# Kernel optimization log

Measured on AMD Instinct MI355X. Metric: run time of the kernel, lower is better.

Reference implementation:

```python
import jax, jax.numpy as jnp
import numpy as np

BS, D, N, E, L, NE = 8, 512, 2048, 8, 64, 524288


def conv1d_same(x, w, b):
    # x: [B, W, Cin], w: [K, Cin, Cout] -> [B, W, Cout], stride 1, 'same' padding
    y = jax.lax.conv_general_dilated(x, w, window_strides=(1,), padding='SAME',
                                     dimension_numbers=('NWC', 'WIO', 'NWC'))
    return y + b


def setup_inputs() -> dict:
    key = jax.random.key(0)
    ks = jax.random.split(key, 10)
    def nrm(k, shape, s=1.0):
        return jax.random.normal(k, shape, jnp.float32) * s
    return {
        'latent': nrm(ks[0], (BS, D)),
        'edge_index': jax.random.randint(ks[1], (2, NE), 0, BS * N),
        'W_dense': nrm(ks[2], (D, N), 0.05),
        'b_dense': jnp.zeros((N,), jnp.float32),
        'conv1_w': nrm(ks[3], (3, 1, E), 0.3),
        'conv1_b': jnp.zeros((E,), jnp.float32),
        'gat_Wq': nrm(ks[4], (E, E), 0.3),
        'gat_bq': jnp.zeros((E,), jnp.float32),
        'gat_Wk': nrm(ks[5], (E, E), 0.3),
        'gat_bk': jnp.zeros((E,), jnp.float32),
        'gat_Wv': nrm(ks[6], (E, E), 0.3),
        'gat_bias': jnp.zeros((E,), jnp.float32),
        'qkv_w': nrm(ks[7], (3, E, 3 * E * L), 0.1),
        'qkv_b': jnp.zeros((3 * E * L,), jnp.float32),
    }


def reference(latent, edge_index, W_dense, b_dense, conv1_w, conv1_b,
              gat_Wq, gat_bq, gat_Wk, gat_bk, gat_Wv, gat_bias, qkv_w, qkv_b):
    bs = latent.shape[0]
    # Dense -> [bs, N], expand -> Conv1D(E) -> [bs, N, E]
    skeleton = latent @ W_dense + b_dense
    skeleton = conv1d_same(skeleton[..., None], conv1_w, conv1_b)
    # concat(unstack, axis=0) == reshape to batched graph nodes [bs*N, E]
    x = skeleton.reshape(bs * N, E)
    BN = bs * N
    # GAT (tf_geometric, num_heads=1): add self-loops, per-edge dot-attention,
    # segment softmax over destination (row), scatter-sum aggregate.
    loops = jnp.arange(BN)
    row = jnp.concatenate([edge_index[0], loops])
    col = jnp.concatenate([edge_index[1], loops])
    Q = jax.nn.leaky_relu(x @ gat_Wq + gat_bq, 0.2)
    K = jax.nn.leaky_relu(x @ gat_Wk + gat_bk, 0.2)
    V = x @ gat_Wv
    score = jnp.sum(Q[row] * K[col], axis=-1)            # [n_edges + BN]
    smax = jax.ops.segment_max(score, row, num_segments=BN)
    ex = jnp.exp(score - smax[row])
    ssum = jax.ops.segment_sum(ex, row, num_segments=BN)
    alpha = ex / ssum[row]                               # segment softmax
    h = jax.ops.segment_sum(alpha[:, None] * V[col], row, num_segments=BN) + gat_bias
    graph = h.reshape(bs, N, E)                          # stack(split(., bs))
    # QVK conv over node axis -> [bs, N, 3*E*L]
    qvk = conv1d_same(graph, qkv_w, qkv_b)
    # stack(split(., L, -1), 1) then concat(unstack(., -2), -1)
    qvk = qvk.reshape(bs, N, L, 3 * E).transpose(0, 2, 1, 3).reshape(bs, L, N * 3 * E)
    q, v, k = jnp.split(qvk, 3, axis=-1)                 # each [bs, L, N*E]
    # keras Attention (use_scale=False): softmax(q @ k^T) @ v
    attn = jax.nn.softmax(jnp.einsum('btd,bsd->bts', q, k), axis=-1)
    seq = jnp.einsum('bts,bsd->btd', attn, v)
    # stack(split(., N, -1), -2) == reshape [bs, L, N, E]
    return seq.reshape(bs, L, N, E)
```

## Files before the change

### kernel.cpp

```cpp
#include <hip/hip_runtime.h>
#include <hip/hip_bf16.h>
#include <math.h>

#define BSZ 8
#define DDIM 512
#define NND 2048
#define EE 8
#define LLH 64
#define NEDGE 524288
#define BNN 16384
#define OCC 1536
#define DQ 16384

typedef __attribute__((ext_vector_type(8))) short short8;
typedef __attribute__((ext_vector_type(4))) unsigned short ushort4v;

__device__ inline unsigned short f2bf(float x) {
    __hip_bfloat16 h = __float2bfloat16(x);
    return __builtin_bit_cast(unsigned short, h);
}
__device__ inline float bf2f(unsigned short u) {
    return __uint_as_float(((unsigned int)u) << 16);
}

__device__ inline void gridbar64(int* c) {
    __syncthreads();
    if (threadIdx.x == 0) {
        __threadfence();
        atomicAdd(c, 1);
        while (atomicAdd(c, 0) < 64) __builtin_amdgcn_s_sleep(8);
        __threadfence();
    }
    __syncthreads();
}

__global__ __launch_bounds__(256) void k_densep(const float* __restrict__ latent,
                                                const float* __restrict__ Wd,
                                                float* __restrict__ pdense,
                                                int* __restrict__ hist,
                                                int* __restrict__ cbar) {
    int n0 = blockIdx.x * 32, d0 = blockIdx.y * 64;
    __shared__ float lat[8][64];
    int tid = threadIdx.x;
    if (blockIdx.y == 0) hist[blockIdx.x * 256 + tid] = 0;
    if (blockIdx.x == 0 && blockIdx.y == 0 && tid < 16) cbar[tid] = 0;
    #pragma unroll
    for (int r = 0; r < 2; ++r) {
        int i = r * 256 + tid;
        lat[i >> 6][i & 63] = latent[(i >> 6) * DDIM + d0 + (i & 63)];
    }
    __syncthreads();
    int nl = tid & 31, b = tid >> 5;
    const float* wp = Wd + (size_t)d0 * NND + n0 + nl;
    float acc = 0.f;
    #pragma unroll 8
    for (int d = 0; d < 64; ++d) acc += lat[b][d] * wp[(size_t)d * NND];
    pdense[((size_t)blockIdx.y * BSZ + b) * NND + n0 + nl] = acc;
}

__global__ __launch_bounds__(64) void k_gat(const float* __restrict__ pdense,
                                            const float* __restrict__ bd,
                                            const float* __restrict__ w1,
                                            const float* __restrict__ b1,
                                            const float* __restrict__ Wq, const float* __restrict__ bq,
                                            const float* __restrict__ Wk, const float* __restrict__ bk,
                                            const float* __restrict__ Wv,
                                            const int* __restrict__ ei,
                                            float* __restrict__ Qg, float* __restrict__ Kg,
                                            float* __restrict__ Vg, int* __restrict__ hist) {
    int i = blockIdx.x * 64 + threadIdx.x;
    int b = i >> 11, n = i & (NND - 1);
    float sm = 0.f, s0 = 0.f, sp = 0.f;
    #pragma unroll
    for (int ds = 0; ds < 8; ++ds) {
        const float* p = pdense + ((size_t)ds * BSZ + b) * NND + n;
        if (n > 0) sm += p[-1];
        s0 += p[0];
        if (n < NND - 1) sp += p[1];
    }
    if (n > 0) sm += bd[n - 1];
    s0 += bd[n];
    if (n < NND - 1) sp += bd[n + 1];
    float xr[EE];
    #pragma unroll
    for (int e = 0; e < EE; ++e)
        xr[e] = sm * w1[e] + s0 * w1[EE + e] + sp * w1[2 * EE + e] + b1[e];
    #pragma unroll
    for (int j = 0; j < EE; ++j) {
        float q = bq[j], k = bk[j], v = 0.f;
        #pragma unroll
        for (int c = 0; c < EE; ++c) {
            q += xr[c] * Wq[c * EE + j];
            k += xr[c] * Wk[c * EE + j];
            v += xr[c] * Wv[c * EE + j];
        }
        Qg[(size_t)i * EE + j] = (q >= 0.f) ? q : 0.2f * q;
        Kg[(size_t)i * EE + j] = (k >= 0.f) ? k : 0.2f * k;
        Vg[(size_t)i * EE + j] = v;
    }
    #pragma unroll 4
    for (int j = 0; j < 32; ++j)
        atomicAdd(hist + ei[i + j * BNN], 1);
}

__global__ __launch_bounds__(1024) void k_scan(const int* __restrict__ hist,
                                               int* __restrict__ offs,
                                               int* __restrict__ cnt) {
    int tid = threadIdx.x;
    int lane = tid & 63, wv = tid >> 6;
    const int4* hp = (const int4*)(hist + tid * 16);
    int4 a = hp[0], b4 = hp[1], c4 = hp[2], d4 = hp[3];
    int h[16] = {a.x, a.y, a.z, a.w, b4.x, b4.y, b4.z, b4.w,
                 c4.x, c4.y, c4.z, c4.w, d4.x, d4.y, d4.z, d4.w};
    int mysum = 0;
    #pragma unroll
    for (int i = 0; i < 16; ++i) mysum += h[i];
    int inc = mysum;
    #pragma unroll
    for (int off = 1; off < 64; off <<= 1) {
        int u = __shfl_up(inc, off, 64);
        if (lane >= off) inc += u;
    }
    __shared__ int wtot[16];
    if (lane == 63) wtot[wv] = inc;
    __syncthreads();
    if (tid < 16) {
        int t = wtot[tid];
        #pragma unroll
        for (int off = 1; off < 16; off <<= 1) {
            int u = __shfl_up(t, off, 16);
            if (tid >= off) t += u;
        }
        wtot[tid] = t;
    }
    __syncthreads();
    int run = (wv ? wtot[wv - 1] : 0) + inc - mysum;
    #pragma unroll
    for (int i = 0; i < 16; ++i) {
        offs[tid * 16 + i] = run;
        cnt[tid * 16 + i] = run;
        run += h[i];
    }
}

__global__ void k_scatter(const int* __restrict__ ei, int* __restrict__ cnt,
                          int* __restrict__ ecol) {
    int e = blockIdx.x * 256 + threadIdx.x;
    if (e >= NEDGE) return;
    int r = ei[e], c = ei[NEDGE + e];
    int pos = atomicAdd(cnt + r, 1);
    ecol[pos] = c;
}

__global__ __launch_bounds__(256) void k_gatagg(const int* __restrict__ ecol,
                                                const int* __restrict__ offs,
                                                const int* __restrict__ hist,
                                                const float* __restrict__ Qg,
                                                const float* __restrict__ Kg,
                                                const float* __restrict__ Vg,
                                                const float* __restrict__ gbias,
                                                float* __restrict__ hg) {
    int row = __builtin_amdgcn_readfirstlane(blockIdx.x * 4 + (threadIdx.x >> 6));
    int lane = threadIdx.x & 63;
    const float* Qr = Qg + (size_t)row * EE;
    float q0 = Qr[0], q1 = Qr[1], q2 = Qr[2], q3 = Qr[3];
    float q4 = Qr[4], q5 = Qr[5], q6 = Qr[6], q7 = Qr[7];
    int beg = offs[row], deg = hist[row];
    int total = deg + 1;
    float m = -INFINITY, l = 0.f;
    float acc[EE];
    #pragma unroll
    for (int j = 0; j < EE; ++j) acc[j] = 0.f;
    for (int base = 0; base < total; base += 64) {
        int idx = base + lane;
        int c = row;
        if (idx < deg) c = ecol[beg + idx];
        const float4* K4 = (const float4*)(Kg + (size_t)c * EE);
        float4 ka = K4[0], kb = K4[1];
        float s = q0*ka.x + q1*ka.y + q2*ka.z + q3*ka.w
                + q4*kb.x + q5*kb.y + q6*kb.z + q7*kb.w;
        if (idx >= total) s = -INFINITY;
        float pm = s;
        #pragma unroll
        for (int off = 32; off > 0; off >>= 1) pm = fmaxf(pm, __shfl_xor(pm, off));
        float nm = fmaxf(m, pm);
        float scale = __expf(m - nm);
        float p = (idx < total) ? __expf(s - nm) : 0.f;
        float ps = p;
        #pragma unroll
        for (int off = 32; off > 0; off >>= 1) ps += __shfl_xor(ps, off);
        l = l * scale + ps;
        const float4* V4 = (const float4*)(Vg + (size_t)c * EE);
        float4 va = V4[0], vb = V4[1];
        float pv[EE] = {p*va.x, p*va.y, p*va.z, p*va.w, p*vb.x, p*vb.y, p*vb.z, p*vb.w};
        #pragma unroll
        for (int j = 0; j < EE; ++j) {
            float t = pv[j];
            #pragma unroll
            for (int off = 32; off > 0; off >>= 1) t += __shfl_xor(t, off);
            acc[j] = acc[j] * scale + t;
        }
        m = nm;
    }
    if (lane < EE)
        hg[(size_t)row * EE + lane] = acc[lane] / l + gbias[lane];
}

__global__ __launch_bounds__(256) void k_midfuse(const float* __restrict__ hg,
                                                 const float* __restrict__ qw,
                                                 const float* __restrict__ qb,
                                                 unsigned short* __restrict__ FvT,
                                                 float* __restrict__ Mpart,
                                                 float* __restrict__ atT,
                                                 int* __restrict__ cbar) {
    __shared__ float smem[16064];
    int bid = blockIdx.x, tid = threadIdx.x;
    if (bid >= 64) {
        int u = bid - 64;
        int cx = u % 22, b = u / 22;
        int n0 = 682 + cx * 32;
        float* hs = smem;
        unsigned short* st = (unsigned short*)(smem + 272);
        for (int i = tid; i < 34 * EE; i += 256) {
            int nn = n0 - 1 + (i >> 3);
            hs[i] = (nn >= 0 && nn < NND) ? hg[((size_t)b * NND + nn) * EE + (i & 7)] : 0.f;
        }
        __syncthreads();
        int dbase = n0 * 24 - DQ;
        #pragma unroll
        for (int pass = 0; pass < 2; ++pass) {
            if (pass) __syncthreads();
            float w[3][24], bias[3];
            #pragma unroll
            for (int rr = 0; rr < 3; ++rr) {
                int o = pass * 768 + rr * 256 + tid;
                bias[rr] = qb[o];
                #pragma unroll
                for (int kk = 0; kk < 24; ++kk) w[rr][kk] = qw[kk * OCC + o];
            }
            for (int nn = 0; nn < 32; ++nn) {
                const float* hv = &hs[nn * EE];
                float a0 = bias[0], a1 = bias[1], a2 = bias[2];
                #pragma unroll
                for (int kk = 0; kk < 24; ++kk) {
                    float h = hv[kk];
                    a0 += h * w[0][kk]; a1 += h * w[1][kk]; a2 += h * w[2][kk];
                }
                st[nn * 768 + tid]       = f2bf(a0);
                st[nn * 768 + tid + 256] = f2bf(a1);
                st[nn * 768 + tid + 512] = f2bf(a2);
            }
            __syncthreads();
            int l0 = pass * 32;
            #pragma unroll
            for (int it = 0; it < 24; ++it) {
                int idx4 = it * 256 + tid;
                int dl = idx4 >> 3, s4 = idx4 & 7;
                int d = dbase + dl;
                if (d < 0 || d >= DQ) continue;
                int nn = dl / 24, c = dl - nn * 24;
                const unsigned short* sb = st + nn * 768 + c;
                ushort4v v4 = { sb[(s4 * 4 + 0) * 24], sb[(s4 * 4 + 1) * 24],
                                sb[(s4 * 4 + 2) * 24], sb[(s4 * 4 + 3) * 24] };
                *(ushort4v*)(FvT + ((size_t)b * DQ + d) * 64 + l0 + s4 * 4) = v4;
            }
        }
    } else {
        int sp = bid >> 3, b = bid & 7;
        int nq0 = sp * 86;
        float* hq = smem;
        float* hk = smem + 704;
        for (int i = tid; i < 88 * EE; i += 256) {
            int r = nq0 - 1 + (i >> 3);
            hq[i] = (r >= 0 && r < NND) ? hg[((size_t)b * NND + r) * EE + (i & 7)] : 0.f;
        }
        for (int i = tid; i < 90 * EE; i += 256) {
            int r = nq0 + 1364 + (i >> 3);
            hk[i] = (r < NND) ? hg[((size_t)b * NND + r) * EE + (i & 7)] : 0.f;
        }
        __syncthreads();
        int cnt1 = 683 - nq0; if (cnt1 > 86) cnt1 = 86; if (cnt1 < 0) cnt1 = 0;
        int cnt2 = 682 - nq0; if (cnt2 > 86) cnt2 = 86; if (cnt2 < 0) cnt2 = 0;
        for (int idx = tid; idx < 1250; idx += 256) {
            int mm = idx / 625, p = idx - (idx / 625) * 625;
            int i = p / 25, j = p - (p / 25) * 25;
            int cnt = mm ? cnt2 : cnt1;
            int qi = i >> 3, qe = i & 7;
            int kj = (j >> 3) + mm, ke = j & 7;
            float acc = 0.f;
            if (i < 24 && j < 24) {
                for (int nl = 0; nl < cnt; ++nl)
                    acc += hq[(nl + qi) * EE + qe] * hk[(nl + kj) * EE + ke];
            } else if (i < 24) {
                for (int nl = 0; nl < cnt; ++nl) acc += hq[(nl + qi) * EE + qe];
            } else if (j < 24) {
                for (int nl = 0; nl < cnt; ++nl) acc += hk[(nl + kj) * EE + ke];
            } else {
                acc = (float)cnt;
            }
            Mpart[((size_t)(sp * 8 + b)) * 1250 + idx] = acc;
        }
        gridbar64(cbar);
        int t = bid;
        float* Ms = smem;
        float* As = smem + 10000;
        float* T1 = smem + 10600;
        for (int idx = tid; idx < 10000; idx += 256) {
            int b2 = idx / 1250, r = idx - (idx / 1250) * 1250;
            float s = 0.f;
            #pragma unroll
            for (int sp2 = 0; sp2 < 8; ++sp2)
                s += Mpart[((size_t)(sp2 * 8 + b2)) * 1250 + r];
            Ms[b2 * 1250 + r] = s;
        }
        for (int idx = tid; idx < 600; idx += 256) {
            int i = idx / 24, c = idx - (idx / 24) * 24;
            As[idx] = (i < 24) ? qw[i * OCC + t * 24 + c] : qb[t * 24 + c];
        }
        __syncthreads();
        for (int idx = tid; idx < 4800; idx += 256) {
            int b2 = idx / 600, rem = idx - (idx / 600) * 600;
            int j = rem / 24, c = rem - (rem / 24) * 24;
            int mo = (c < 16) ? 0 : 625;
            float acc = 0.f;
            #pragma unroll 5
            for (int i = 0; i < 25; ++i)
                acc += Ms[b2 * 1250 + mo + i * 25 + j] * As[i * 24 + c];
            T1[b2 * 600 + j * 24 + c] = acc;
        }
        __syncthreads();
        int s = tid & 63, bg = tid >> 6;
        float acc0 = 0.f, acc1 = 0.f;
        for (int j = 0; j < 25; ++j) {
            float Bv[24];
            const float* bp = (j < 24) ? (qw + (size_t)j * OCC + s * 24) : (qb + s * 24);
            #pragma unroll
            for (int r = 0; r < 6; ++r) {
                float4 v = *(const float4*)(bp + r * 4);
                Bv[r*4+0]=v.x; Bv[r*4+1]=v.y; Bv[r*4+2]=v.z; Bv[r*4+3]=v.w;
            }
            const float* t1a = &T1[bg * 600 + j * 24];
            const float* t1b = &T1[(bg + 4) * 600 + j * 24];
            #pragma unroll
            for (int c = 0; c < 16; ++c) {
                acc0 += t1a[c] * Bv[8 + c];
                acc1 += t1b[c] * Bv[8 + c];
            }
            #pragma unroll
            for (int c = 16; c < 24; ++c) {
                acc0 += t1a[c] * Bv[c - 16];
                acc1 += t1b[c] * Bv[c - 16];
            }
        }
        #pragma unroll
        for (int r = 0; r < 2; ++r) {
            int b2 = bg + r * 4;
            float v = r ? acc1 : acc0;
            float m = v;
            #pragma unroll
            for (int off = 32; off > 0; off >>= 1) m = fmaxf(m, __shfl_xor(m, off));
            float e = __expf(v - m);
            float sum = e;
            #pragma unroll
            for (int off = 32; off > 0; off >>= 1) sum += __shfl_xor(sum, off);
            atT[((size_t)b2 * LLH + s) * LLH + t] = e / sum;
        }
    }
}

__global__ __launch_bounds__(256) void k_attnV(const unsigned short* __restrict__ FvT,
                                               const float* __restrict__ atT,
                                               float* __restrict__ out) {
    int b = blockIdx.y;
    int d0 = blockIdx.x * 64;
    int tid = threadIdx.x;
    __shared__ float vtf[64][65];
    #pragma unroll
    for (int r = 0; r < 2; ++r) {
        int idx = r * 256 + tid;
        int dl = idx >> 3, g = idx & 7;
        short8 v = *(const short8*)(FvT + ((size_t)b * DQ + d0 + dl) * 64 + g * 8);
        #pragma unroll
        for (int j = 0; j < 8; ++j)
            vtf[dl][g * 8 + j] = bf2f((unsigned short)v[j]);
    }
    __syncthreads();
    int lane = tid & 63;
    int t0 = __builtin_amdgcn_readfirstlane((tid >> 6) * 16);
    const float* arow = atT + (size_t)b * LLH * LLH + t0;
    float acc[16];
    #pragma unroll
    for (int tt = 0; tt < 16; ++tt) acc[tt] = 0.f;
    #pragma unroll 4
    for (int s = 0; s < LLH; ++s) {
        float vv = vtf[lane][s];
        #pragma unroll
        for (int tt = 0; tt < 16; ++tt)
            acc[tt] += arow[s * LLH + tt] * vv;
    }
    float* ob = out + ((size_t)b * LLH + t0) * DQ + d0 + lane;
    #pragma unroll
    for (int tt = 0; tt < 16; ++tt) ob[(size_t)tt * DQ] = acc[tt];
}

extern "C" void kernel_launch(void* const* d_in, const int* in_sizes, int n_in,
                              void* d_out, int out_size, void* d_ws, size_t ws_size,
                              hipStream_t stream) {
    (void)in_sizes; (void)n_in; (void)out_size; (void)ws_size;
    const float* latent = (const float*)d_in[0];
    const int*   ei     = (const int*)d_in[1];
    const float* Wd     = (const float*)d_in[2];
    const float* bd     = (const float*)d_in[3];
    const float* w1     = (const float*)d_in[4];
    const float* b1     = (const float*)d_in[5];
    const float* Wq     = (const float*)d_in[6];
    const float* bq     = (const float*)d_in[7];
    const float* Wk     = (const float*)d_in[8];
    const float* bk     = (const float*)d_in[9];
    const float* Wv     = (const float*)d_in[10];
    const float* gbias  = (const float*)d_in[11];
    const float* qw     = (const float*)d_in[12];
    const float* qb     = (const float*)d_in[13];
    float* out = (float*)d_out;

    float* ws     = (float*)d_ws;
    float* pdense = ws;
    float* Qg     = pdense + 64 * NND;
    float* Kg     = Qg + BNN * EE;
    float* Vg     = Kg + BNN * EE;
    float* hg     = Vg + BNN * EE;
    int*   hist   = (int*)(hg + BNN * EE);
    int*   offs   = hist + BNN;
    int*   cnt    = offs + BNN;
    int*   ecol   = cnt + BNN;
    int*   cbar   = ecol + NEDGE;
    float* Mp     = (float*)(cbar + 16);
    float* atT    = Mp + 80000;
    unsigned short* FvT = (unsigned short*)(atT + BSZ * LLH * LLH);

    k_densep<<<dim3(64, 8), dim3(256), 0, stream>>>(latent, Wd, pdense, hist, cbar);
    k_gat<<<dim3(256), dim3(64), 0, stream>>>(pdense, bd, w1, b1, Wq, bq, Wk, bk, Wv,
                                              ei, Qg, Kg, Vg, hist);
    k_scan<<<dim3(1), dim3(1024), 0, stream>>>(hist, offs, cnt);
    k_scatter<<<dim3(NEDGE / 256), dim3(256), 0, stream>>>(ei, cnt, ecol);
    k_gatagg<<<dim3(BNN / 4), dim3(256), 0, stream>>>(ecol, offs, hist,
                                                      Qg, Kg, Vg, gbias, hg);
    k_midfuse<<<dim3(240), dim3(256), 0, stream>>>(hg, qw, qb, FvT, Mp, atT, cbar);
    k_attnV<<<dim3(256, 8), dim3(256), 0, stream>>>(FvT, atT, out);
}
```

Measured before the change: 147.3 us.

## Split fused mid kernel into separate V-conv and attention-matrix kernels

```diff
diff --git a/kernel.cpp b/kernel.cpp
--- a/kernel.cpp
+++ b/kernel.cpp
@@ -206,66 +206,71 @@
         hg[(size_t)row * EE + lane] = acc[lane] / l + gbias[lane];
 }
 
-__global__ __launch_bounds__(256) void k_midfuse(const float* __restrict__ hg,
-                                                 const float* __restrict__ qw,
-                                                 const float* __restrict__ qb,
-                                                 unsigned short* __restrict__ FvT,
-                                                 float* __restrict__ Mpart,
-                                                 float* __restrict__ atT,
-                                                 int* __restrict__ cbar) {
-    __shared__ float smem[16064];
+__global__ __launch_bounds__(256) void k_convV(const float* __restrict__ hg,
+                                               const float* __restrict__ qw,
+                                               const float* __restrict__ qb,
+                                               unsigned short* __restrict__ FvT) {
+    int cx = blockIdx.x, b = blockIdx.y;
+    int n0 = 682 + cx * 8;
+    __shared__ float hs[10 * EE];
+    __shared__ unsigned short st[8 * 768];
+    int tid = threadIdx.x;
+    for (int i = tid; i < 10 * EE; i += 256) {
+        int nn = n0 - 1 + (i >> 3);
+        hs[i] = (nn < NND) ? hg[((size_t)b * NND + nn) * EE + (i & 7)] : 0.f;
+    }
+    __syncthreads();
+    int dbase = n0 * 24 - DQ;
+    #pragma unroll
+    for (int pass = 0; pass < 2; ++pass) {
+        if (pass) __syncthreads();
+        float w[3][24], bias[3];
+        #pragma unroll
+        for (int rr = 0; rr < 3; ++rr) {
+            int o = pass * 768 + rr * 256 + tid;
+            bias[rr] = qb[o];
+            #pragma unroll
+            for (int kk = 0; kk < 24; ++kk) w[rr][kk] = qw[kk * OCC + o];
+        }
+        #pragma unroll
+        for (int nn = 0; nn < 8; ++nn) {
+            const float* hv = &hs[nn * EE];
+            float a0 = bias[0], a1 = bias[1], a2 = bias[2];
+            #pragma unroll
+            for (int kk = 0; kk < 24; ++kk) {
+                float h = hv[kk];
+                a0 += h * w[0][kk]; a1 += h * w[1][kk]; a2 += h * w[2][kk];
+            }
+            st[nn * 768 + tid]       = f2bf(a0);
+            st[nn * 768 + tid + 256] = f2bf(a1);
+            st[nn * 768 + tid + 512] = f2bf(a2);
+        }
+        __syncthreads();
+        int l0 = pass * 32;
+        #pragma unroll
+        for (int it = 0; it < 6; ++it) {
+            int idx = it * 256 + tid;
+            int dl = idx >> 3, s4 = idx & 7;
+            int d = dbase + dl;
+            if (d < 0 || d >= DQ) continue;
+            int nn = dl / 24, c = dl - nn * 24;
+            const unsigned short* sb = st + nn * 768 + c;
+            ushort4v v4 = { sb[(s4 * 4 + 0) * 24], sb[(s4 * 4 + 1) * 24],
+                            sb[(s4 * 4 + 2) * 24], sb[(s4 * 4 + 3) * 24] };
+            *(ushort4v*)(FvT + ((size_t)b * DQ + d) * 64 + l0 + s4 * 4) = v4;
+        }
+    }
+}
+
+__global__ __launch_bounds__(256) void k_MSsm(const float* __restrict__ hg,
+                                              const float* __restrict__ qw,
+                                              const float* __restrict__ qb,
+                                              float* __restrict__ Mpart,
+                                              float* __restrict__ atT,
+                                              int* __restrict__ cbar) {
+    __shared__ float smem[15400];
     int bid = blockIdx.x, tid = threadIdx.x;
-    if (bid >= 64) {
-        int u = bid - 64;
-        int cx = u % 22, b = u / 22;
-        int n0 = 682 + cx * 32;
-        float* hs = smem;
-        unsigned short* st = (unsigned short*)(smem + 272);
-        for (int i = tid; i < 34 * EE; i += 256) {
-            int nn = n0 - 1 + (i >> 3);
-            hs[i] = (nn >= 0 && nn < NND) ? hg[((size_t)b * NND + nn) * EE + (i & 7)] : 0.f;
-        }
-        __syncthreads();
-        int dbase = n0 * 24 - DQ;
-        #pragma unroll
-        for (int pass = 0; pass < 2; ++pass) {
-            if (pass) __syncthreads();
-            float w[3][24], bias[3];
-            #pragma unroll
-            for (int rr = 0; rr < 3; ++rr) {
-                int o = pass * 768 + rr * 256 + tid;
-                bias[rr] = qb[o];
-                #pragma unroll
-                for (int kk = 0; kk < 24; ++kk) w[rr][kk] = qw[kk * OCC + o];
-            }
-            for (int nn = 0; nn < 32; ++nn) {
-                const float* hv = &hs[nn * EE];
-                float a0 = bias[0], a1 = bias[1], a2 = bias[2];
-                #pragma unroll
-                for (int kk = 0; kk < 24; ++kk) {
-                    float h = hv[kk];
-                    a0 += h * w[0][kk]; a1 += h * w[1][kk]; a2 += h * w[2][kk];
-                }
-                st[nn * 768 + tid]       = f2bf(a0);
-                st[nn * 768 + tid + 256] = f2bf(a1);
-                st[nn * 768 + tid + 512] = f2bf(a2);
-            }
-            __syncthreads();
-            int l0 = pass * 32;
-            #pragma unroll
-            for (int it = 0; it < 24; ++it) {
-                int idx4 = it * 256 + tid;
-                int dl = idx4 >> 3, s4 = idx4 & 7;
-                int d = dbase + dl;
-                if (d < 0 || d >= DQ) continue;
-                int nn = dl / 24, c = dl - nn * 24;
-                const unsigned short* sb = st + nn * 768 + c;
-                ushort4v v4 = { sb[(s4 * 4 + 0) * 24], sb[(s4 * 4 + 1) * 24],
-                                sb[(s4 * 4 + 2) * 24], sb[(s4 * 4 + 3) * 24] };
-                *(ushort4v*)(FvT + ((size_t)b * DQ + d) * 64 + l0 + s4 * 4) = v4;
-            }
-        }
-    } else {
+    {
         int sp = bid >> 3, b = bid & 7;
         int nq0 = sp * 86;
         float* hq = smem;
@@ -300,7 +305,9 @@
             }
             Mpart[((size_t)(sp * 8 + b)) * 1250 + idx] = acc;
         }
-        gridbar64(cbar);
+    }
+    gridbar64(cbar);
+    {
         int t = bid;
         float* Ms = smem;
         float* As = smem + 10000;
@@ -445,6 +452,7 @@
     k_scatter<<<dim3(NEDGE / 256), dim3(256), 0, stream>>>(ei, cnt, ecol);
     k_gatagg<<<dim3(BNN / 4), dim3(256), 0, stream>>>(ecol, offs, hist,
                                                       Qg, Kg, Vg, gbias, hg);
-    k_midfuse<<<dim3(240), dim3(256), 0, stream>>>(hg, qw, qb, FvT, Mp, atT, cbar);
+    k_convV<<<dim3(86, 8), dim3(256), 0, stream>>>(hg, qw, qb, FvT);
+    k_MSsm<<<dim3(64), dim3(256), 0, stream>>>(hg, qw, qb, Mp, atT, cbar);
     k_attnV<<<dim3(256, 8), dim3(256), 0, stream>>>(FvT, atT, out);
 }
```

Result: slower. 160.1 us (+8.7%).
